# Kernel tuning notes

Measured on AMD Instinct MI355X. Metric: run time of the kernel, lower is better.

The kernel has to match this reference:

```python
import jax, jax.numpy as jnp
import numpy as np

N_RNA, N_DIS = 40000, 3000
E_EDGES, T = 600000, 10000
RNA_IN, D_FEAT, HID, EXP_D = 512, 256, 512, 256
N_EXP, HEADS = 8, 8
HD = HID // HEADS          # per-head dim inside HANConv
MHA_HD = EXP_D // HEADS    # per-head dim in cross-attention
FUSION = 2 * HID


def setup_inputs() -> dict:
    key = jax.random.key(0)
    ks = iter(jax.random.split(key, 48))
    def nrm(shape, s=0.02):
        return jax.random.normal(next(ks), shape, dtype=jnp.float32) * s
    inp = {
        "x_rna": jax.random.normal(next(ks), (N_RNA, RNA_IN), dtype=jnp.float32),
        "x_dis": jax.random.normal(next(ks), (N_DIS, D_FEAT), dtype=jnp.float32),
        "Wd": nrm((RNA_IN, D_FEAT)), "bd": jnp.zeros((RNA_IN,), jnp.float32),
        "Wp_r": nrm((HID, RNA_IN)), "bp_r": jnp.zeros((HID,), jnp.float32),
        "Wp_d": nrm((HID, RNA_IN)), "bp_d": jnp.zeros((HID,), jnp.float32),
        "a_src_rd": nrm((HEADS, HD), 0.1), "a_dst_rd": nrm((HEADS, HD), 0.1),
        "a_src_dr": nrm((HEADS, HD), 0.1), "a_dst_dr": nrm((HEADS, HD), 0.1),
        "kW": nrm((HID, HID)), "kb": jnp.zeros((HID,), jnp.float32),
        "qv": nrm((HID,), 0.1),
        "Wl": nrm((HID, HID)), "bl": jnp.zeros((HID,), jnp.float32),
        "W_exp": nrm((N_EXP, FUSION, EXP_D)), "b_exp": jnp.zeros((N_EXP, EXP_D), jnp.float32),
        "W_gate": nrm((4, HID, N_EXP)),
        "W_head": nrm((4, 2 * EXP_D, EXP_D)), "b_head": jnp.zeros((4, EXP_D), jnp.float32),
        "in_w": nrm((3 * EXP_D, EXP_D)), "in_b": jnp.zeros((3 * EXP_D,), jnp.float32),
        "out_w": nrm((EXP_D, EXP_D)), "out_b": jnp.zeros((EXP_D,), jnp.float32),
        "Wdp": nrm((EXP_D, HID)), "bdp": jnp.zeros((EXP_D,), jnp.float32),
        "ei_rd_src": jax.random.randint(next(ks), (E_EDGES,), 0, N_RNA),
        "ei_rd_dst": jax.random.randint(next(ks), (E_EDGES,), 0, N_DIS),
        "ei_dr_src": jax.random.randint(next(ks), (E_EDGES,), 0, N_DIS),
        "ei_dr_dst": jax.random.randint(next(ks), (E_EDGES,), 0, N_RNA),
        "idx_rels": jax.random.randint(next(ks), (4, T), 0, N_RNA),
    }
    return inp


def _han_edge(x_src, x_dst, ei_src, ei_dst, a_src, a_dst, n_dst):
    # x_*: [N, H, D]; GAT-style attention with softmax per destination node (PyG HANConv edge step)
    as_ = (x_src * a_src).sum(-1)                                 # [Ns, H]
    ad_ = (x_dst * a_dst).sum(-1)                                 # [Nd, H]
    alpha = jax.nn.leaky_relu(as_[ei_src] + ad_[ei_dst], 0.2)     # [E, H]
    amax = jax.ops.segment_max(alpha, ei_dst, num_segments=n_dst)
    ex = jnp.exp(alpha - amax[ei_dst])
    den = jax.ops.segment_sum(ex, ei_dst, num_segments=n_dst)
    w = ex / (den[ei_dst] + 1e-16)
    msg = x_src[ei_src] * w[:, :, None]                           # [E, H, D]
    out = jax.ops.segment_sum(msg, ei_dst, num_segments=n_dst)    # [Nd, H, D]
    return jax.nn.relu(out.reshape(n_dst, -1))


def _semantic(outs, kW, kb, qv):
    # outs: [M, N, F]; metapath-level (semantic) attention from HANConv
    s = (jnp.tanh(outs @ kW.T + kb).mean(axis=1) * qv).sum(-1)    # [M]
    beta = jax.nn.softmax(s)
    return (beta[:, None, None] * outs).sum(0)


def reference(x_rna, x_dis, Wd, bd, Wp_r, bp_r, Wp_d, bp_d,
              a_src_rd, a_dst_rd, a_src_dr, a_dst_dr,
              kW, kb, qv, Wl, bl, W_exp, b_exp, W_gate, W_head, b_head,
              in_w, in_b, out_w, out_b, Wdp, bdp,
              ei_rd_src, ei_rd_dst, ei_dr_src, ei_dr_dst, idx_rels):
    # ---- HAN encoder ----
    xd = x_dis @ Wd.T + bd                                        # disease feat -> rna_in_dim
    hr0 = (x_rna @ Wp_r.T + bp_r).reshape(N_RNA, HEADS, HD)
    hd0 = (xd @ Wp_d.T + bp_d).reshape(N_DIS, HEADS, HD)
    out_dis = _han_edge(hr0, hd0, ei_rd_src, ei_rd_dst, a_src_rd, a_dst_rd, N_DIS)
    out_rna = _han_edge(hd0, hr0, ei_dr_src, ei_dr_dst, a_src_dr, a_dst_dr, N_RNA)
    h_rna = _semantic(out_rna[None], kW, kb, qv) @ Wl.T + bl      # shared final lin
    h_dis = _semantic(out_dis[None], kW, kb, qv) @ Wl.T + bl
    # ---- MoE with per-relation gating ----
    d_global = h_dis.mean(axis=0)
    fusion = jnp.concatenate([h_rna, jnp.broadcast_to(d_global, h_rna.shape)], axis=1)  # [N, 2H]
    E = jax.nn.relu(jnp.einsum('nf,efd->ned', fusion, W_exp) + b_exp)  # [N, Nexp, Ed]
    h_t = h_rna[idx_rels]                                         # [4, T, H]
    scores = jnp.einsum('rth,rhe->rte', h_t, W_gate)              # raw gate scores (no softmax)
    u = (E[idx_rels] * scores[..., None]).sum(axis=2)             # [4, T, Ed]
    U = u.mean(axis=1)                                            # [4, Ed]
    # ---- cross attention over 4 task tokens ----
    qkv = U @ in_w.T + in_b
    q, k, v = jnp.split(qkv, 3, axis=-1)
    def heads(z):
        return z.reshape(4, HEADS, MHA_HD).transpose(1, 0, 2)     # [H, 4, dh]
    qh, kh, vh = heads(q), heads(k), heads(v)
    attn = jax.nn.softmax(jnp.einsum('htd,hsd->hts', qh, kh) / np.float32(np.sqrt(MHA_HD)), axis=-1)
    o = jnp.einsum('hts,hsd->htd', attn, vh).transpose(1, 0, 2).reshape(4, EXP_D)
    U_prime = o @ out_w.T + out_b                                 # [4, Ed]
    # ---- per-relation heads and disease scores ----
    cross = jnp.broadcast_to(U_prime[:, None, :], u.shape)
    cat = jnp.concatenate([u, cross], axis=-1)                    # [4, T, 2Ed]
    p = jax.nn.relu(jnp.einsum('rtc,rcd->rtd', cat, W_head) + b_head[:, None, :])
    d_proj = h_dis @ Wdp.T + bdp                                  # [Ndis, Ed]
    return jax.nn.sigmoid(jnp.einsum('rtd,md->rtm', p, d_proj))   # [4, T, Ndis]
```

## Files before the change

### kernel.cpp

```cpp
#include <hip/hip_runtime.h>
#include <math.h>

constexpr int NRNA = 40000;
constexpr int NDIS = 3000;
constexpr int NEDG = 600000;
constexpr int TREL = 10000;

typedef __attribute__((ext_vector_type(8))) short bh8;
typedef __attribute__((ext_vector_type(4))) float f32x4;

__device__ inline float bf2f(ushort x) {
    union { uint u; float f; } v; v.u = ((uint)x) << 16; return v.f;
}
__device__ inline ushort f2bf(float f) {
    union { float f; uint u; } v; v.f = f;
    uint u = v.u;
    uint r = (u + 0x7fffu + ((u >> 16) & 1u)) >> 16;
    return (ushort)r;
}
__device__ inline float bflo(uint w) { union { uint u; float f; } v; v.u = w << 16; return v.f; }
__device__ inline float bfhi(uint w) { union { uint u; float f; } v; v.u = w & 0xffff0000u; return v.f; }

__device__ inline void gload16(const ushort* g, ushort* l) {
    __builtin_amdgcn_global_load_lds(
        (const __attribute__((address_space(1))) unsigned int*)(const void*)g,
        (__attribute__((address_space(3))) unsigned int*)(void*)l, 16, 0, 0);
}

__device__ inline int xcd_swz(int f, int n) {
    int q = n >> 3, r = n & 7, xcd = f & 7, i = f >> 3;
    return (xcd < r) ? (xcd * (q + 1) + i) : (r * (q + 1) + (xcd - r) * q + i);
}

__global__ __launch_bounds__(256) void conv_bf16(const float* __restrict__ in,
                                                 ushort* __restrict__ out, long n)
{
    long g = ((long)blockIdx.x * 256 + threadIdx.x) * 4;
    if (g >= n) return;
    float4 v = *(const float4*)(in + g);
    ushort4 o;
    o.x = f2bf(v.x); o.y = f2bf(v.y); o.z = f2bf(v.z); o.w = f2bf(v.w);
    *(ushort4*)(out + g) = o;
}

__global__ __launch_bounds__(256) void transpose_bf16(
    const float* __restrict__ in, ushort* __restrict__ out,
    int R, int C, long sIn, long sOut)
{
    __shared__ float t[64][65];
    const int tid = threadIdx.x;
    const int r0 = blockIdx.y * 64, c0 = blockIdx.x * 64;
    const float* ib = in + (long)blockIdx.z * sIn;
    ushort* ob = out + (long)blockIdx.z * sOut;
#pragma unroll
    for (int k = 0; k < 16; ++k) {
        int idx = k * 256 + tid, i = idx >> 6, j = idx & 63;
        t[i][j] = ib[(long)(r0 + i) * C + c0 + j];
    }
    __syncthreads();
#pragma unroll
    for (int k = 0; k < 16; ++k) {
        int idx = k * 256 + tid, i = idx >> 6, j = idx & 63;
        ob[(long)(c0 + i) * R + r0 + j] = f2bf(t[j][i]);
    }
}

__global__ void transpose_wgate(const float* __restrict__ W, float* __restrict__ out)
{
    int g = blockIdx.x * 256 + threadIdx.x;
    int r = g >> 12, e = (g >> 9) & 7, k = g & 511;
    out[g] = W[(long)r * 4096 + (long)k * 8 + e];
}

template<int ACT, bool SWZ>
__global__ __launch_bounds__(256) void gemm_mfma(
    const ushort* __restrict__ A, const ushort* __restrict__ B,
    const float* __restrict__ bias, float* __restrict__ Cf, ushort* __restrict__ Cb,
    const int* __restrict__ idx,
    int M, int N, int K, long sA, long sB, long sBias, long sC)
{
    __shared__ ushort smem[16384];
    ushort* As = smem;
    ushort* Bs = smem + 8192;
    int bx = blockIdx.x, by = blockIdx.y;
    if (SWZ) {
        int n = gridDim.x * gridDim.y;
        int s = xcd_swz(by * gridDim.x + bx, n);
        bx = s % gridDim.x; by = s / gridDim.x;
    }
    const int bz = blockIdx.z;
    const ushort* Ab = A + (long)bz * sA;
    const ushort* Bb = B + (long)bz * sB;
    const float* biasb = bias ? (bias + (long)bz * sBias) : nullptr;
    const int row0 = by * 128, col0 = bx * 128;

    const int tid = threadIdx.x, wid = tid >> 6, lane = tid & 63;
    const int wr = wid >> 1, wc = wid & 1;

    const int lrow = lane >> 3;
    const int lk = (((lane & 7) ^ lrow) * 8);
    const ushort* ap0[4]; const ushort* bp0[4];
    ushort* la[4]; ushort* lb[4];
#pragma unroll
    for (int i = 0; i < 4; ++i) {
        int c = wid * 4 + i;
        int ra = row0 + c * 8 + lrow; ra = ra < M ? ra : M - 1;
        int rs = idx ? idx[ra] : ra;
        ap0[i] = Ab + (long)rs * K + lk;
        int cb = col0 + c * 8 + lrow; cb = cb < N ? cb : N - 1;
        bp0[i] = Bb + (long)cb * K + lk;
        la[i] = As + c * 512;
        lb[i] = Bs + c * 512;
    }

    f32x4 acc[4][4];
#pragma unroll
    for (int i = 0; i < 4; ++i)
#pragma unroll
        for (int n = 0; n < 4; ++n) acc[i][n] = (f32x4){0.f, 0.f, 0.f, 0.f};

    const int fr = lane & 15, fq = lane >> 4;
    const int sw0 = (fq ^ (fr & 7)) * 8;
    const ushort* paRow = As + (wr * 64 + fr) * 64;
    const ushort* pbRow = Bs + (wc * 64 + fr) * 64;

    for (int k0 = 0; k0 < K; k0 += 64) {
#pragma unroll
        for (int i = 0; i < 4; ++i) gload16(ap0[i] + k0, la[i]);
#pragma unroll
        for (int i = 0; i < 4; ++i) gload16(bp0[i] + k0, lb[i]);
        __syncthreads();
#pragma unroll
        for (int kk = 0; kk < 2; ++kk) {
            const int sw = kk ? (sw0 ^ 32) : sw0;
            bh8 af[4], bf[4];
#pragma unroll
            for (int i = 0; i < 4; ++i) af[i] = *(const bh8*)(paRow + i * 1024 + sw);
#pragma unroll
            for (int n = 0; n < 4; ++n) bf[n] = *(const bh8*)(pbRow + n * 1024 + sw);
#pragma unroll
            for (int i = 0; i < 4; ++i)
#pragma unroll
                for (int n = 0; n < 4; ++n)
                    acc[i][n] = __builtin_amdgcn_mfma_f32_16x16x32_bf16(af[i], bf[n], acc[i][n], 0, 0, 0);
        }
        __syncthreads();
    }

    float* cs = (float*)smem;
#pragma unroll
    for (int H = 0; H < 2; ++H) {
        if (wc == H) {
#pragma unroll
            for (int i = 0; i < 4; ++i)
#pragma unroll
                for (int n = 0; n < 4; ++n)
#pragma unroll
                    for (int r = 0; r < 4; ++r)
                        cs[(wr * 64 + i * 16 + fq * 4 + r) * 64 + n * 16 + fr] = acc[i][n][r];
        }
        __syncthreads();
#pragma unroll
        for (int it = 0; it < 8; ++it) {
            int rl = it * 16 + (tid >> 4);
            int cl = (tid & 15) * 4;
            int m = row0 + rl, col = col0 + H * 64 + cl;
            if (m < M && col < N) {
                f32x4 v = *(const f32x4*)(cs + rl * 64 + cl);
                if (biasb) {
                    float4 bv = *(const float4*)(biasb + col);
                    v[0] += bv.x; v[1] += bv.y; v[2] += bv.z; v[3] += bv.w;
                }
                if (ACT == 1) {
#pragma unroll
                    for (int q = 0; q < 4; ++q) v[q] = fmaxf(v[q], 0.f);
                } else if (ACT == 2) {
#pragma unroll
                    for (int q = 0; q < 4; ++q) v[q] = 1.f / (1.f + __expf(-v[q]));
                }
                long o = (long)bz * sC + (long)m * N + col;
                if (Cf) *(f32x4*)(Cf + o) = v;
                if (Cb) {
                    ushort4 ob;
                    ob.x = f2bf(v[0]); ob.y = f2bf(v[1]); ob.z = f2bf(v[2]); ob.w = f2bf(v[3]);
                    *(ushort4*)(Cb + o) = ob;
                }
            }
        }
        __syncthreads();
    }
}

__global__ __launch_bounds__(256) void moe_mfma(
    const ushort* __restrict__ h, const ushort* __restrict__ WexpT,
    const float* __restrict__ c_exp, const float* __restrict__ S,
    const int* __restrict__ idx, ushort* __restrict__ up)
{
    __shared__ ushort smem[24576];
    __shared__ float sS[128 * 2];
    __shared__ float sC[2 * 128];
    ushort* As  = smem;
    ushort* Bs0 = smem + 8192;
    ushort* Bs1 = smem + 16384;
    int bx = blockIdx.x, by = blockIdx.y;
    {
        int n = gridDim.x * gridDim.y;
        int s = xcd_swz(by * gridDim.x + bx, n);
        bx = s % gridDim.x; by = s / gridDim.x;
    }
    const int row0 = by * 128, col0 = bx * 128;
    const int z = blockIdx.z, e0 = z * 2;
    const int tid = threadIdx.x, wid = tid >> 6, lane = tid & 63;
    const int wr = wid >> 1, wc = wid & 1;
    constexpr int M = 4 * TREL;

    {
        int rr = tid >> 1, e = tid & 1;
        sS[tid] = S[(long)(row0 + rr) * 8 + e0 + e];
        int ee = tid >> 7, cc = tid & 127;
        sC[tid] = c_exp[(e0 + ee) * 256 + col0 + cc];
    }

    const int lrow = lane >> 3;
    const int lk = (((lane & 7) ^ lrow) * 8);
    const ushort* ap0[4]; const ushort* bp0[4];
    ushort* la[4]; ushort* lb0[4]; ushort* lb1[4];
#pragma unroll
    for (int i = 0; i < 4; ++i) {
        int c = wid * 4 + i;
        int ra = row0 + c * 8 + lrow;
        ap0[i] = h + (long)idx[ra] * 512 + lk;
        bp0[i] = WexpT + (long)(col0 + c * 8 + lrow) * 512 + (long)e0 * 131072 + lk;
        la[i]  = As  + c * 512;
        lb0[i] = Bs0 + c * 512;
        lb1[i] = Bs1 + c * 512;
    }

    const int fr = lane & 15, fq = lane >> 4;
    const int sw0 = (fq ^ (fr & 7)) * 8;
    const ushort* paRow  = As  + (wr * 64 + fr) * 64;
    const ushort* pb0Row = Bs0 + (wc * 64 + fr) * 64;
    const ushort* pb1Row = Bs1 + (wc * 64 + fr) * 64;

    f32x4 acc0[4][4], acc1[4][4];
#pragma unroll
    for (int i = 0; i < 4; ++i)
#pragma unroll
        for (int n = 0; n < 4; ++n) {
            acc0[i][n] = (f32x4){0.f, 0.f, 0.f, 0.f};
            acc1[i][n] = (f32x4){0.f, 0.f, 0.f, 0.f};
        }
    __syncthreads();

    for (int k0 = 0; k0 < 512; k0 += 64) {
#pragma unroll
        for (int i = 0; i < 4; ++i) gload16(ap0[i] + k0, la[i]);
#pragma unroll
        for (int i = 0; i < 4; ++i) gload16(bp0[i] + k0, lb0[i]);
#pragma unroll
        for (int i = 0; i < 4; ++i) gload16(bp0[i] + 131072 + k0, lb1[i]);
        __syncthreads();
#pragma unroll
        for (int kk = 0; kk < 2; ++kk) {
            const int sw = kk ? (sw0 ^ 32) : sw0;
            bh8 af[4], b0[4], b1[4];
#pragma unroll
            for (int i = 0; i < 4; ++i) af[i] = *(const bh8*)(paRow + i * 1024 + sw);
#pragma unroll
            for (int n = 0; n < 4; ++n) b0[n] = *(const bh8*)(pb0Row + n * 1024 + sw);
#pragma unroll
            for (int n = 0; n < 4; ++n) b1[n] = *(const bh8*)(pb1Row + n * 1024 + sw);
#pragma unroll
            for (int i = 0; i < 4; ++i)
#pragma unroll
                for (int n = 0; n < 4; ++n) {
                    acc0[i][n] = __builtin_amdgcn_mfma_f32_16x16x32_bf16(af[i], b0[n], acc0[i][n], 0, 0, 0);
                    acc1[i][n] = __builtin_amdgcn_mfma_f32_16x16x32_bf16(af[i], b1[n], acc1[i][n], 0, 0, 0);
                }
        }
        __syncthreads();
    }

#pragma unroll
    for (int i = 0; i < 4; ++i) {
        int rl = wr * 64 + i * 16 + fq * 4;
#pragma unroll
        for (int n = 0; n < 4; ++n) {
            int cl = wc * 64 + n * 16 + fr;
            float c0 = sC[cl], c1 = sC[128 + cl];
#pragma unroll
            for (int r = 0; r < 4; ++r) {
                float s0 = sS[(rl + r) * 2 + 0];
                float s1 = sS[(rl + r) * 2 + 1];
                acc0[i][n][r] = s0 * fmaxf(acc0[i][n][r] + c0, 0.f)
                              + s1 * fmaxf(acc1[i][n][r] + c1, 0.f);
            }
        }
    }

    float* cs = (float*)smem;
    ushort* upz = up + (long)z * M * 256;
#pragma unroll
    for (int H = 0; H < 2; ++H) {
        if (wc == H) {
#pragma unroll
            for (int i = 0; i < 4; ++i)
#pragma unroll
                for (int n = 0; n < 4; ++n)
#pragma unroll
                    for (int r = 0; r < 4; ++r)
                        cs[(wr * 64 + i * 16 + fq * 4 + r) * 64 + n * 16 + fr] = acc0[i][n][r];
        }
        __syncthreads();
#pragma unroll
        for (int it = 0; it < 8; ++it) {
            int rl = it * 16 + (tid >> 4);
            int cl = (tid & 15) * 4;
            f32x4 v = *(const f32x4*)(cs + rl * 64 + cl);
            int m = row0 + rl, col = col0 + H * 64 + cl;
            ushort4 ob;
            ob.x = f2bf(v[0]); ob.y = f2bf(v[1]); ob.z = f2bf(v[2]); ob.w = f2bf(v[3]);
            *(ushort4*)(upz + (long)m * 256 + col) = ob;
        }
        __syncthreads();
    }
}

__global__ __launch_bounds__(256) void moe_combine(const ushort* __restrict__ up,
                                                   ushort* __restrict__ u)
{
    constexpr long TOT = (long)4 * TREL * 256;
    long g = ((long)blockIdx.x * 256 + threadIdx.x) * 4;
    if (g >= TOT) return;
    float a[4] = {0.f, 0.f, 0.f, 0.f};
#pragma unroll
    for (int z = 0; z < 4; ++z) {
        ushort4 v = *(const ushort4*)(up + z * TOT + g);
        a[0] += bf2f(v.x); a[1] += bf2f(v.y); a[2] += bf2f(v.z); a[3] += bf2f(v.w);
    }
    ushort4 o;
    o.x = f2bf(a[0]); o.y = f2bf(a[1]); o.z = f2bf(a[2]); o.w = f2bf(a[3]);
    *(ushort4*)(u + g) = o;
}

__global__ void dot_heads_all(const ushort* __restrict__ xr, const ushort* __restrict__ xd,
                              const float* __restrict__ a_src_rd, const float* __restrict__ a_dst_dr,
                              const float* __restrict__ a_dst_rd, const float* __restrict__ a_src_dr,
                              float* __restrict__ as_rd, float* __restrict__ ad_dr,
                              float* __restrict__ ad_rd, float* __restrict__ as_dr)
{
    long g = (long)blockIdx.x * 256 + threadIdx.x;
    const ushort* x; const float *p1, *p2; float *o1, *o2; long gi;
    if (g < (long)NRNA * 8) {
        gi = g; x = xr; p1 = a_src_rd; p2 = a_dst_dr; o1 = as_rd; o2 = ad_dr;
    } else {
        gi = g - (long)NRNA * 8;
        if (gi >= (long)NDIS * 8) return;
        x = xd; p1 = a_dst_rd; p2 = a_src_dr; o1 = ad_rd; o2 = as_dr;
    }
    int node = (int)(gi >> 3), h = (int)(gi & 7);
    const ushort* xp = x + (long)node * 512 + h * 64;
    const float* q1 = p1 + h * 64;
    const float* q2 = p2 + h * 64;
    float s1 = 0.f, s2 = 0.f;
#pragma unroll
    for (int d = 0; d < 64; d += 8) {
        uint4 xv = *(const uint4*)(xp + d);
        float xf[8] = { bflo(xv.x), bfhi(xv.x), bflo(xv.y), bfhi(xv.y),
                        bflo(xv.z), bfhi(xv.z), bflo(xv.w), bfhi(xv.w) };
#pragma unroll
        for (int j = 0; j < 8; ++j) {
            s1 = fmaf(xf[j], q1[d + j], s1);
            s2 = fmaf(xf[j], q2[d + j], s2);
        }
    }
    o1[gi] = s1; o2[gi] = s2;
}

__global__ void hist2(const int* __restrict__ d0, int* __restrict__ deg0,
                      const int* __restrict__ d1, int* __restrict__ deg1, int E)
{
    int g = blockIdx.x * 256 + threadIdx.x;
    if (g >= E) return;
    if (blockIdx.y == 0) atomicAdd(&deg0[d0[g]], 1);
    else                 atomicAdd(&deg1[d1[g]], 1);
}

__global__ __launch_bounds__(1024) void scan_blocks2(
    const int* __restrict__ in0, int* __restrict__ tmp0, int* __restrict__ bs0, int n0,
    const int* __restrict__ in1, int* __restrict__ tmp1, int* __restrict__ bs1, int n1)
{
    const int z = blockIdx.y;
    const int* in = z ? in1 : in0;
    int* tmp = z ? tmp1 : tmp0;
    int* bsum = z ? bs1 : bs0;
    const int n = z ? n1 : n0;
    const int nb = (n + 1023) >> 10;
    if ((int)blockIdx.x >= nb) return;
    __shared__ int wsum[16];
    const int tid = threadIdx.x, lane = tid & 63, wid = tid >> 6;
    int base = blockIdx.x * 1024;
    int v = (base + tid < n) ? in[base + tid] : 0;
    int s = v;
#pragma unroll
    for (int off = 1; off < 64; off <<= 1) {
        int t = __shfl_up(s, off, 64);
        if (lane >= off) s += t;
    }
    if (lane == 63) wsum[wid] = s;
    __syncthreads();
    if (wid == 0) {
        int w = (lane < 16) ? wsum[lane] : 0;
#pragma unroll
        for (int off = 1; off < 16; off <<= 1) {
            int t = __shfl_up(w, off, 64);
            if (lane >= off) w += t;
        }
        if (lane < 16) wsum[lane] = w;
    }
    __syncthreads();
    int incl = s + ((wid == 0) ? 0 : wsum[wid - 1]);
    if (base + tid < n) tmp[base + tid] = incl;
    if (tid == 1023) bsum[blockIdx.x] = incl;
}

__global__ void scan_bsums2(int* __restrict__ bs0, int nb0, int* __restrict__ bs1, int nb1)
{
    int* bsum = blockIdx.x ? bs1 : bs0;
    int nb = blockIdx.x ? nb1 : nb0;
    int lane = threadIdx.x;
    int v = (lane < nb) ? bsum[lane] : 0;
#pragma unroll
    for (int off = 1; off < 64; off <<= 1) {
        int t = __shfl_up(v, off, 64);
        if (lane >= off) v += t;
    }
    if (lane < nb) bsum[lane] = v;
}

__global__ __launch_bounds__(1024) void scan_finish2(
    const int* __restrict__ in0, const int* __restrict__ tmp0, const int* __restrict__ bs0,
    int* __restrict__ offs0, int* __restrict__ cur0, int n0,
    const int* __restrict__ in1, const int* __restrict__ tmp1, const int* __restrict__ bs1,
    int* __restrict__ offs1, int* __restrict__ cur1, int n1)
{
    const int z = blockIdx.y;
    const int* in = z ? in1 : in0;
    const int* tmp = z ? tmp1 : tmp0;
    const int* bsum = z ? bs1 : bs0;
    int* offs = z ? offs1 : offs0;
    int* cur = z ? cur1 : cur0;
    const int n = z ? n1 : n0;
    const int nb = (n + 1023) >> 10;
    if ((int)blockIdx.x >= nb) return;
    int base = blockIdx.x * 1024;
    int i = base + threadIdx.x;
    if (i < n) {
        int pre = (blockIdx.x == 0) ? 0 : bsum[blockIdx.x - 1];
        int v = tmp[i] - in[i] + pre;
        offs[i] = v;
        cur[i] = v;
    }
    if (i == 0) offs[n] = bsum[nb - 1];
}

__global__ void scatter2(const int* __restrict__ s0, const int* __restrict__ d0,
                         int* __restrict__ c0, int* __restrict__ o0,
                         const int* __restrict__ s1, const int* __restrict__ d1,
                         int* __restrict__ c1, int* __restrict__ o1, int E)
{
    int g = blockIdx.x * 256 + threadIdx.x;
    if (g >= E) return;
    if (blockIdx.y == 0) {
        int p = atomicAdd(&c0[d0[g]], 1);
        o0[p] = s0[g];
    } else {
        int p = atomicAdd(&c1[d1[g]], 1);
        o1[p] = s1[g];
    }
}

__global__ __launch_bounds__(256) void han_wave(
    const int* __restrict__ offs, const int* __restrict__ csr_src,
    const float* __restrict__ as_, const float* __restrict__ ad_,
    const ushort* __restrict__ x_src, ushort* __restrict__ out, int nnode)
{
    __shared__ float s_ex[4][64];
    __shared__ int   s_src[4][8];
    __shared__ float s_den[4][8];
    const int w = threadIdx.x >> 6, lane = threadIdx.x & 63;
    const int node = blockIdx.x * 4 + w;
    if (node >= nnode) return;
    const int e0 = offs[node], ne = offs[node + 1] - e0;
    const int myh = lane & 7, grp = lane >> 3;
    const float my_ad = ad_[node * 8 + myh];

    float den = 0.f;
    float acc[8];
#pragma unroll
    for (int k = 0; k < 8; ++k) acc[k] = 0.f;
    const int colbase = lane * 8;

    for (int c0 = 0; c0 < ne; c0 += 8) {
        const int nc = min(8, ne - c0);
        float ex = 0.f;
        int src = 0;
        if (grp < nc) {
            src = csr_src[e0 + c0 + grp];
            float al = as_[(long)src * 8 + myh] + my_ad;
            al = al >= 0.f ? al : 0.2f * al;
            ex = __expf(al);
            den += ex;
        }
        s_ex[w][grp * 8 + myh] = ex;
        if (myh == 0) s_src[w][grp] = src;
        asm volatile("s_waitcnt lgkmcnt(0)" ::: "memory");
        for (int j = 0; j < nc; ++j) {
            float wg = s_ex[w][j * 8 + grp];
            uint4 xv = *(const uint4*)(x_src + (long)s_src[w][j] * 512 + colbase);
            acc[0] = fmaf(wg, bflo(xv.x), acc[0]);
            acc[1] = fmaf(wg, bfhi(xv.x), acc[1]);
            acc[2] = fmaf(wg, bflo(xv.y), acc[2]);
            acc[3] = fmaf(wg, bfhi(xv.y), acc[3]);
            acc[4] = fmaf(wg, bflo(xv.z), acc[4]);
            acc[5] = fmaf(wg, bfhi(xv.z), acc[5]);
            acc[6] = fmaf(wg, bflo(xv.w), acc[6]);
            acc[7] = fmaf(wg, bfhi(xv.w), acc[7]);
        }
        __builtin_amdgcn_wave_barrier();
    }

#pragma unroll
    for (int m = 8; m < 64; m <<= 1) den += __shfl_xor(den, m, 64);
    if (grp == 0) s_den[w][myh] = den;
    asm volatile("s_waitcnt lgkmcnt(0)" ::: "memory");
    float d = s_den[w][grp] + 1e-16f;

    uint4 ov;
    ov.x = (uint)f2bf(fmaxf(acc[0] / d, 0.f)) | ((uint)f2bf(fmaxf(acc[1] / d, 0.f)) << 16);
    ov.y = (uint)f2bf(fmaxf(acc[2] / d, 0.f)) | ((uint)f2bf(fmaxf(acc[3] / d, 0.f)) << 16);
    ov.z = (uint)f2bf(fmaxf(acc[4] / d, 0.f)) | ((uint)f2bf(fmaxf(acc[5] / d, 0.f)) << 16);
    ov.w = (uint)f2bf(fmaxf(acc[6] / d, 0.f)) | ((uint)f2bf(fmaxf(acc[7] / d, 0.f)) << 16);
    *(uint4*)(out + (long)node * 512 + colbase) = ov;
}

__global__ __launch_bounds__(512) void hdis_colsum_partial(const ushort* __restrict__ h_dis,
                                                           float* __restrict__ part)
{
    int c = blockIdx.x, d = threadIdx.x;
    int r0 = c * 200;
    float s = 0.f;
    for (int r = r0; r < r0 + 200; ++r) s += bf2f(h_dis[(long)r * 512 + d]);
    part[c * 512 + d] = s;
}
__global__ __launch_bounds__(512) void hdis_colsum_finish(const float* __restrict__ part,
                                                          float* __restrict__ dg)
{
    int d = threadIdx.x;
    float s = 0.f;
    for (int c = 0; c < 15; ++c) s += part[c * 512 + d];
    dg[d] = s * (1.f / NDIS);
}

__global__ void cexp_part(const float* __restrict__ dg, const float* __restrict__ W_exp,
                          float* __restrict__ part)
{
    int b = blockIdx.x;
    int e = b >> 3, ch = b & 7, d = threadIdx.x;
    const float* W = W_exp + (long)e * 262144 + (long)(512 + ch * 64) * 256 + d;
    float s = 0.f;
    for (int f = 0; f < 64; ++f) s = fmaf(dg[ch * 64 + f], W[(long)f * 256], s);
    part[b * 256 + d] = s;
}
__global__ void cexp_fin(const float* __restrict__ part, const float* __restrict__ b_exp,
                         float* __restrict__ c_exp)
{
    int e = blockIdx.x, d = threadIdx.x;
    float s = b_exp[e * 256 + d];
    for (int ch = 0; ch < 8; ++ch) s += part[(e * 8 + ch) * 256 + d];
    c_exp[e * 256 + d] = s;
}

__global__ __launch_bounds__(256) void scores2(const ushort* __restrict__ h,
                                               const float* __restrict__ WgT,
                                               const int* __restrict__ idx,
                                               float* __restrict__ S)
{
    __shared__ float sW[8 * 512];
    const int r = blockIdx.y;
    const int tid = threadIdx.x;
    for (int i = tid; i < 4096; i += 256) sW[i] = WgT[(long)r * 4096 + i];
    __syncthreads();
    int n = blockIdx.x * 256 + tid;
    if (n >= TREL) return;
    int gi = r * TREL + n;
    const ushort* hp = h + (long)idx[gi] * 512;
    float acc[8];
#pragma unroll
    for (int e = 0; e < 8; ++e) acc[e] = 0.f;
    for (int k = 0; k < 512; k += 8) {
        uint4 hv = *(const uint4*)(hp + k);
        float hf[8];
        hf[0] = bflo(hv.x); hf[1] = bfhi(hv.x); hf[2] = bflo(hv.y); hf[3] = bfhi(hv.y);
        hf[4] = bflo(hv.z); hf[5] = bfhi(hv.z); hf[6] = bflo(hv.w); hf[7] = bfhi(hv.w);
#pragma unroll
        for (int e = 0; e < 8; ++e)
#pragma unroll
            for (int j = 0; j < 8; ++j)
                acc[e] = fmaf(hf[j], sW[e * 512 + k + j], acc[e]);
    }
#pragma unroll
    for (int e = 0; e < 8; ++e) S[(long)gi * 8 + e] = acc[e];
}

__global__ void u_mean_partial(const ushort* __restrict__ u, float* __restrict__ part)
{
    int c = blockIdx.x, r = blockIdx.y, d = threadIdx.x;
    int t0 = c * 313, t1 = min(t0 + 313, TREL);
    const ushort* base = u + ((long)r * TREL) * 256 + d;
    float s = 0.f;
    for (int t = t0; t < t1; ++t) s += bf2f(base[(long)t * 256]);
    part[((long)r * 32 + c) * 256 + d] = s;
}

__global__ __launch_bounds__(256) void tail_kernel(
    const float* __restrict__ u_part,
    const float* __restrict__ in_w, const float* __restrict__ in_b,
    const float* __restrict__ out_w, const float* __restrict__ out_b,
    const float* __restrict__ W_head, const float* __restrict__ b_head,
    float* __restrict__ c_head)
{
    __shared__ float sU[4 * 256];
    __shared__ float sqkv[4 * 768];
    __shared__ float sattn[128];
    __shared__ float so[4 * 256];
    __shared__ float sUp[4 * 256];
    const int tid = threadIdx.x;

    for (int o = tid; o < 1024; o += 256) {
        int r = o >> 8, d = o & 255;
        float s = 0.f;
        for (int c = 0; c < 32; ++c) s += u_part[((long)r * 32 + c) * 256 + d];
        sU[o] = s * (1.f / TREL);
    }
    __syncthreads();

    for (int o = tid; o < 3072; o += 256) {
        int row = o / 768, col = o % 768;
        const float* w = in_w + (long)col * 256;
        const float* uu = sU + row * 256;
        float s = in_b[col];
        for (int k = 0; k < 256; ++k) s = fmaf(uu[k], w[k], s);
        sqkv[o] = s;
    }
    __syncthreads();
    if (tid < 128) {
        int h = tid >> 4, t = (tid >> 2) & 3, s2 = tid & 3;
        const float* q = sqkv + t * 768 + h * 32;
        const float* kk = sqkv + s2 * 768 + 256 + h * 32;
        float s = 0.f;
        for (int d = 0; d < 32; ++d) s += q[d] * kk[d];
        sattn[tid] = s * 0.17677669529663687f;
    }
    __syncthreads();
    if (tid < 32) {
        int base = tid * 4;
        float a0 = sattn[base], a1 = sattn[base+1], a2 = sattn[base+2], a3 = sattn[base+3];
        float m = fmaxf(fmaxf(a0, a1), fmaxf(a2, a3));
        float e0 = __expf(a0 - m), e1 = __expf(a1 - m), e2 = __expf(a2 - m), e3 = __expf(a3 - m);
        float inv = 1.f / (e0 + e1 + e2 + e3);
        sattn[base] = e0 * inv; sattn[base+1] = e1 * inv;
        sattn[base+2] = e2 * inv; sattn[base+3] = e3 * inv;
    }
    __syncthreads();
    for (int o = tid; o < 1024; o += 256) {
        int t = o >> 8, hd = o & 255, h = hd >> 5, d = hd & 31;
        const float* a = sattn + (h * 4 + t) * 4;
        float s = 0.f;
        for (int s2 = 0; s2 < 4; ++s2) s += a[s2] * sqkv[s2 * 768 + 512 + h * 32 + d];
        so[t * 256 + hd] = s;
    }
    __syncthreads();
    for (int o = tid; o < 1024; o += 256) {
        int t = o >> 8, d = o & 255;
        const float* w = out_w + (long)d * 256;
        const float* ov = so + t * 256;
        float s = out_b[d];
        for (int k = 0; k < 256; ++k) s = fmaf(ov[k], w[k], s);
        sUp[o] = s;
    }
    __syncthreads();

    for (int o = tid; o < 1024; o += 256) {
        int r = o >> 8, d = o & 255;
        const float* W = W_head + (long)r * 131072 + 65536 + d;
        const float* up = sUp + r * 256;
        float s = b_head[o];
        for (int c = 0; c < 256; ++c) s = fmaf(up[c], W[(long)c * 256], s);
        c_head[o] = s;
    }
}

extern "C" void kernel_launch(void* const* d_in, const int* in_sizes, int n_in,
                              void* d_out, int out_size, void* d_ws, size_t ws_size,
                              hipStream_t stream)
{
    (void)in_sizes; (void)n_in; (void)out_size;
    const float* x_rna    = (const float*)d_in[0];
    const float* x_dis    = (const float*)d_in[1];
    const float* Wd       = (const float*)d_in[2];
    const float* bd       = (const float*)d_in[3];
    const float* Wp_r     = (const float*)d_in[4];
    const float* bp_r     = (const float*)d_in[5];
    const float* Wp_d     = (const float*)d_in[6];
    const float* bp_d     = (const float*)d_in[7];
    const float* a_src_rd = (const float*)d_in[8];
    const float* a_dst_rd = (const float*)d_in[9];
    const float* a_src_dr = (const float*)d_in[10];
    const float* a_dst_dr = (const float*)d_in[11];
    const float* Wl       = (const float*)d_in[15];
    const float* bl       = (const float*)d_in[16];
    const float* W_exp    = (const float*)d_in[17];
    const float* b_exp    = (const float*)d_in[18];
    const float* W_gate   = (const float*)d_in[19];
    const float* W_head   = (const float*)d_in[20];
    const float* b_head   = (const float*)d_in[21];
    const float* in_w     = (const float*)d_in[22];
    const float* in_b     = (const float*)d_in[23];
    const float* out_w    = (const float*)d_in[24];
    const float* out_b    = (const float*)d_in[25];
    const float* Wdp      = (const float*)d_in[26];
    const float* bdp      = (const float*)d_in[27];
    const int* ei_rd_src  = (const int*)d_in[28];
    const int* ei_rd_dst  = (const int*)d_in[29];
    const int* ei_dr_src  = (const int*)d_in[30];
    const int* ei_dr_dst  = (const int*)d_in[31];
    const int* idx_rels   = (const int*)d_in[32];
    float* out = (float*)d_out;

    char* ws = (char*)d_ws;
    size_t off = 0;
    auto alloc = [&](size_t bytes) -> void* {
        off = (off + 255) & ~(size_t)255;
        void* p = ws + off;
        off += bytes;
        return p;
    };
    constexpr int NALL = NRNA + NDIS;
    ushort* xrb      = (ushort*)alloc((size_t)NRNA * 512 * 2);
    ushort* hr0b     = (ushort*)alloc((size_t)NRNA * 512 * 2);
    ushort* out_all  = (ushort*)alloc((size_t)(NALL + 8) * 512 * 2);
    ushort* h_all    = (ushort*)alloc((size_t)(NALL + 8) * 512 * 2);
    ushort* u_bf     = (ushort*)alloc((size_t)4 * TREL * 256 * 2);
    ushort* p_bf     = (ushort*)alloc((size_t)4 * TREL * 256 * 2);
    ushort* up_bf    = (ushort*)alloc((size_t)4 * 4 * TREL * 256 * 2);
    ushort* xdb      = (ushort*)alloc((size_t)NDIS * 256 * 2);
    ushort* xd_bf    = (ushort*)alloc((size_t)NDIS * 512 * 2);
    ushort* hd0b     = (ushort*)alloc((size_t)NDIS * 512 * 2);
    ushort* dproj_b  = (ushort*)alloc((size_t)NDIS * 256 * 2);
    ushort* Wdb    = (ushort*)alloc((size_t)512 * 256 * 2);
    ushort* Wprb   = (ushort*)alloc((size_t)512 * 512 * 2);
    ushort* Wpdb   = (ushort*)alloc((size_t)512 * 512 * 2);
    ushort* Wlb    = (ushort*)alloc((size_t)512 * 512 * 2);
    ushort* Wdpb   = (ushort*)alloc((size_t)256 * 512 * 2);
    ushort* WexpT  = (ushort*)alloc((size_t)8 * 256 * 512 * 2);
    ushort* WheadT = (ushort*)alloc((size_t)4 * 256 * 256 * 2);
    float*  WgT    = (float*)alloc((size_t)4 * 8 * 512 * 4);
    float* as_rd   = (float*)alloc((size_t)NRNA * 8 * 4);
    float* ad_rd   = (float*)alloc((size_t)NDIS * 8 * 4);
    float* as_dr   = (float*)alloc((size_t)NDIS * 8 * 4);
    float* ad_dr   = (float*)alloc((size_t)NRNA * 8 * 4);
    float* S       = (float*)alloc((size_t)4 * TREL * 8 * 4);
    float* dg_part = (float*)alloc((size_t)15 * 512 * 4);
    float* dg      = (float*)alloc((size_t)512 * 4);
    float* c_exp   = (float*)alloc((size_t)8 * 256 * 4);
    float* ce_part = (float*)alloc((size_t)64 * 256 * 4);
    float* u_part  = (float*)alloc((size_t)4 * 32 * 256 * 4);
    float* c_head  = (float*)alloc((size_t)4 * 256 * 4);
    int* deg_all  = (int*)alloc((size_t)(NDIS + NRNA) * 4);
    int* deg_rd = deg_all, * deg_dr = deg_all + NDIS;
    int* offs_rd = (int*)alloc((size_t)(NDIS + 1) * 4);
    int* cur_rd  = (int*)alloc((size_t)NDIS * 4);
    int* csr_rd  = (int*)alloc((size_t)NEDG * 4);
    int* offs_dr = (int*)alloc((size_t)(NRNA + 1) * 4);
    int* cur_dr  = (int*)alloc((size_t)NRNA * 4);
    int* csr_dr  = (int*)alloc((size_t)NEDG * 4);
    int* tmp_rd  = (int*)alloc((size_t)NDIS * 4);
    int* tmp_dr  = (int*)alloc((size_t)NRNA * 4);
    int* bs_rd   = (int*)alloc((size_t)64 * 4);
    int* bs_dr   = (int*)alloc((size_t)64 * 4);
    if (off > ws_size) return;

    ushort* out_rna = out_all;
    ushort* out_dis = out_all + (size_t)NRNA * 512;
    ushort* h_rna   = h_all;
    ushort* h_dis   = h_all + (size_t)NRNA * 512;

    const dim3 blk(256);

    conv_bf16<<<dim3(20000), blk, 0, stream>>>(x_rna, xrb, (long)NRNA * 512);
    conv_bf16<<<dim3(750),   blk, 0, stream>>>(x_dis, xdb, (long)NDIS * 256);
    conv_bf16<<<dim3(128),   blk, 0, stream>>>(Wd,   Wdb,  512 * 256);
    conv_bf16<<<dim3(256),   blk, 0, stream>>>(Wp_r, Wprb, 512 * 512);
    conv_bf16<<<dim3(256),   blk, 0, stream>>>(Wp_d, Wpdb, 512 * 512);
    conv_bf16<<<dim3(256),   blk, 0, stream>>>(Wl,   Wlb,  512 * 512);
    conv_bf16<<<dim3(128),   blk, 0, stream>>>(Wdp,  Wdpb, 256 * 512);
    transpose_bf16<<<dim3(4, 8, 8), blk, 0, stream>>>(W_exp, WexpT, 512, 256,
                                                      (long)1024 * 256, (long)256 * 512);
    transpose_bf16<<<dim3(4, 4, 4), blk, 0, stream>>>(W_head, WheadT, 256, 256,
                                                      (long)512 * 256, (long)256 * 256);
    transpose_wgate<<<dim3(64), blk, 0, stream>>>(W_gate, WgT);

    gemm_mfma<0,false><<<dim3(4, 24), blk, 0, stream>>>(
        xdb, Wdb, bd, nullptr, xd_bf, nullptr, NDIS, 512, 256, 0, 0, 0, 0);
    gemm_mfma<0,true><<<dim3(4, 313), blk, 0, stream>>>(
        xrb, Wprb, bp_r, nullptr, hr0b, nullptr, NRNA, 512, 512, 0, 0, 0, 0);
    gemm_mfma<0,false><<<dim3(4, 24), blk, 0, stream>>>(
        xd_bf, Wpdb, bp_d, nullptr, hd0b, nullptr, NDIS, 512, 512, 0, 0, 0, 0);

    dot_heads_all<<<dim3(((NRNA + NDIS) * 8 + 255) / 256), blk, 0, stream>>>(
        hr0b, hd0b, a_src_rd, a_dst_dr, a_dst_rd, a_src_dr, as_rd, ad_dr, ad_rd, as_dr);

    hipMemsetAsync(deg_all, 0, (size_t)(NDIS + NRNA) * 4, stream);
    hist2<<<dim3((NEDG + 255) / 256, 2), blk, 0, stream>>>(ei_rd_dst, deg_rd, ei_dr_dst, deg_dr, NEDG);
    scan_blocks2<<<dim3(40, 2), dim3(1024), 0, stream>>>(deg_rd, tmp_rd, bs_rd, NDIS,
                                                         deg_dr, tmp_dr, bs_dr, NRNA);
    scan_bsums2<<<dim3(2), dim3(64), 0, stream>>>(bs_rd, 3, bs_dr, 40);
    scan_finish2<<<dim3(40, 2), dim3(1024), 0, stream>>>(deg_rd, tmp_rd, bs_rd, offs_rd, cur_rd, NDIS,
                                                         deg_dr, tmp_dr, bs_dr, offs_dr, cur_dr, NRNA);
    scatter2<<<dim3((NEDG + 255) / 256, 2), blk, 0, stream>>>(
        ei_rd_src, ei_rd_dst, cur_rd, csr_rd, ei_dr_src, ei_dr_dst, cur_dr, csr_dr, NEDG);

    han_wave<<<dim3((NDIS + 3) / 4), blk, 0, stream>>>(offs_rd, csr_rd, as_rd, ad_rd, hr0b, out_dis, NDIS);
    han_wave<<<dim3(NRNA / 4), blk, 0, stream>>>(offs_dr, csr_dr, as_dr, ad_dr, hd0b, out_rna, NRNA);

    gemm_mfma<0,true><<<dim3(4, (NALL + 127) / 128), blk, 0, stream>>>(
        out_all, Wlb, bl, nullptr, h_all, nullptr, NALL, 512, 512, 0, 0, 0, 0);

    hdis_colsum_partial<<<dim3(15), dim3(512), 0, stream>>>(h_dis, dg_part);
    hdis_colsum_finish<<<dim3(1), dim3(512), 0, stream>>>(dg_part, dg);
    cexp_part<<<dim3(64), blk, 0, stream>>>(dg, W_exp, ce_part);
    cexp_fin<<<dim3(8), blk, 0, stream>>>(ce_part, b_exp, c_exp);
    scores2<<<dim3(40, 4), blk, 0, stream>>>(h_rna, WgT, idx_rels, S);

    moe_mfma<<<dim3(2, 320, 4), blk, 0, stream>>>(h_rna, WexpT, c_exp, S, idx_rels, up_bf);
    moe_combine<<<dim3(10240), blk, 0, stream>>>(up_bf, u_bf);

    u_mean_partial<<<dim3(32, 4), blk, 0, stream>>>(u_bf, u_part);
    tail_kernel<<<dim3(1), blk, 0, stream>>>(u_part, in_w, in_b, out_w, out_b,
                                             W_head, b_head, c_head);

    gemm_mfma<1,false><<<dim3(2, 79, 4), blk, 0, stream>>>(
        u_bf, WheadT, c_head, nullptr, p_bf, nullptr, TREL, 256, 256,
        (long)TREL * 256, 65536, 256, (long)TREL * 256);

    gemm_mfma<0,false><<<dim3(2, 24), blk, 0, stream>>>(
        h_dis, Wdpb, bdp, nullptr, dproj_b, nullptr, NDIS, 256, 512, 0, 0, 0, 0);

    gemm_mfma<2,true><<<dim3(24, 320), blk, 0, stream>>>(
        p_bf, dproj_b, nullptr, out, nullptr, nullptr, 4 * TREL, NDIS, 256, 0, 0, 0, 0);
}
```

Baseline: 1.271 ms.

## Merge small launches and fold disease linear layers into one weight

Several small kernels are merged into single launches: the six fp32-to-bf16 conversions, the two HAN aggregation passes, the gate scores with the disease column sums, and the relation-head GEMM with the disease projection GEMM. The two chained disease linear layers are algebraically folded into one precomputed 512x256 weight plus a combined bias, so the disease projection runs over K=256 once instead of two GEMMs. The aim is to cut launch overhead and small-kernel tail waste. The cost is branchy block dispatch and extra bf16 rounding on the folded weight.

```diff
diff --git a/kernel.cpp b/kernel.cpp
--- a/kernel.cpp
+++ b/kernel.cpp
@@ -32,15 +32,25 @@
     return (xcd < r) ? (xcd * (q + 1) + i) : (r * (q + 1) + (xcd - r) * q + i);
 }
 
-__global__ __launch_bounds__(256) void conv_bf16(const float* __restrict__ in,
-                                                 ushort* __restrict__ out, long n)
-{
-    long g = ((long)blockIdx.x * 256 + threadIdx.x) * 4;
-    if (g >= n) return;
-    float4 v = *(const float4*)(in + g);
+__global__ __launch_bounds__(256) void conv_multi(
+    const float* s0, ushort* d0, const float* s1, ushort* d1,
+    const float* s2, ushort* d2, const float* s3, ushort* d3,
+    const float* s4, ushort* d4, const float* s5, ushort* d5,
+    int c0, int c1, int c2, int c3, int c4, int c5)
+{
+    int b = blockIdx.x;
+    const float* src; ushort* dst; int base;
+    if      (b < c0) { src = s0; dst = d0; base = 0;  }
+    else if (b < c1) { src = s1; dst = d1; base = c0; }
+    else if (b < c2) { src = s2; dst = d2; base = c1; }
+    else if (b < c3) { src = s3; dst = d3; base = c2; }
+    else if (b < c4) { src = s4; dst = d4; base = c3; }
+    else             { src = s5; dst = d5; base = c4; }
+    long g = ((long)(b - base) * 256 + threadIdx.x) * 4;
+    float4 v = *(const float4*)(src + g);
     ushort4 o;
     o.x = f2bf(v.x); o.y = f2bf(v.y); o.z = f2bf(v.z); o.w = f2bf(v.w);
-    *(ushort4*)(out + g) = o;
+    *(ushort4*)(dst + g) = o;
 }
 
 __global__ __launch_bounds__(256) void transpose_bf16(
@@ -72,23 +82,28 @@
     out[g] = W[(long)r * 4096 + (long)k * 8 + e];
 }
 
-template<int ACT, bool SWZ>
-__global__ __launch_bounds__(256) void gemm_mfma(
+__global__ __launch_bounds__(256) void bias_fold(
+    const float* __restrict__ Wp_d, const float* __restrict__ bd,
+    const float* __restrict__ bp_d, float* __restrict__ bias_comb)
+{
+    int p = blockIdx.x * 256 + threadIdx.x;
+    const float* W = Wp_d + (long)p * 512;
+    float s = bp_d[p];
+    for (int o = 0; o < 512; ++o) s = fmaf(W[o], bd[o], s);
+    bias_comb[p] = s;
+}
+
+template<int ACT>
+__device__ inline void gemm_body(
+    ushort* smem,
     const ushort* __restrict__ A, const ushort* __restrict__ B,
     const float* __restrict__ bias, float* __restrict__ Cf, ushort* __restrict__ Cb,
     const int* __restrict__ idx,
-    int M, int N, int K, long sA, long sB, long sBias, long sC)
-{
-    __shared__ ushort smem[16384];
+    int M, int N, int K, long sA, long sB, long sBias, long sC,
+    int bx, int by, int bz)
+{
     ushort* As = smem;
     ushort* Bs = smem + 8192;
-    int bx = blockIdx.x, by = blockIdx.y;
-    if (SWZ) {
-        int n = gridDim.x * gridDim.y;
-        int s = xcd_swz(by * gridDim.x + bx, n);
-        bx = s % gridDim.x; by = s / gridDim.x;
-    }
-    const int bz = blockIdx.z;
     const ushort* Ab = A + (long)bz * sA;
     const ushort* Bb = B + (long)bz * sB;
     const float* biasb = bias ? (bias + (long)bz * sBias) : nullptr;
@@ -188,6 +203,43 @@
             }
         }
         __syncthreads();
+    }
+}
+
+template<int ACT, bool SWZ>
+__global__ __launch_bounds__(256) void gemm_mfma(
+    const ushort* __restrict__ A, const ushort* __restrict__ B,
+    const float* __restrict__ bias, float* __restrict__ Cf, ushort* __restrict__ Cb,
+    const int* __restrict__ idx,
+    int M, int N, int K, long sA, long sB, long sBias, long sC)
+{
+    __shared__ ushort smem[16384];
+    int bx = blockIdx.x, by = blockIdx.y;
+    if (SWZ) {
+        int n = gridDim.x * gridDim.y;
+        int s = xcd_swz(by * gridDim.x + bx, n);
+        bx = s % gridDim.x; by = s / gridDim.x;
+    }
+    gemm_body<ACT>(smem, A, B, bias, Cf, Cb, idx, M, N, K, sA, sB, sBias, sC,
+                   bx, by, blockIdx.z);
+}
+
+__global__ __launch_bounds__(256) void gemm_two(
+    const ushort* __restrict__ u, const ushort* __restrict__ WheadT,
+    const float* __restrict__ c_head, ushort* __restrict__ p,
+    const ushort* __restrict__ h_dis, const ushort* __restrict__ Wdpb,
+    const float* __restrict__ bdp, ushort* __restrict__ dproj)
+{
+    __shared__ ushort smem[16384];
+    const int z = blockIdx.z;
+    if (z < 4) {
+        gemm_body<1>(smem, u, WheadT, c_head, nullptr, p, nullptr,
+                     TREL, 256, 256, (long)TREL * 256, 65536, 256, (long)TREL * 256,
+                     blockIdx.x, blockIdx.y, z);
+    } else if (blockIdx.y < 24) {
+        gemm_body<0>(smem, h_dis, Wdpb, bdp, nullptr, dproj, nullptr,
+                     NDIS, 256, 512, 0, 0, 0, 0,
+                     blockIdx.x, blockIdx.y, 0);
     }
 }
 
@@ -480,16 +532,28 @@
     }
 }
 
-__global__ __launch_bounds__(256) void han_wave(
-    const int* __restrict__ offs, const int* __restrict__ csr_src,
-    const float* __restrict__ as_, const float* __restrict__ ad_,
-    const ushort* __restrict__ x_src, ushort* __restrict__ out, int nnode)
-{
+__global__ __launch_bounds__(256) void han_both(
+    const int* __restrict__ offs_rd, const int* __restrict__ csr_rd,
+    const float* __restrict__ as_rd, const float* __restrict__ ad_rd,
+    const ushort* __restrict__ x_rd, ushort* __restrict__ out_rd,
+    const int* __restrict__ offs_dr, const int* __restrict__ csr_dr,
+    const float* __restrict__ as_dr, const float* __restrict__ ad_dr,
+    const ushort* __restrict__ x_dr, ushort* __restrict__ out_dr)
+{
+    constexpr int NB_RD = (NDIS + 3) / 4;
     __shared__ float s_ex[4][64];
     __shared__ int   s_src[4][8];
     __shared__ float s_den[4][8];
     const int w = threadIdx.x >> 6, lane = threadIdx.x & 63;
-    const int node = blockIdx.x * 4 + w;
+    const int* offs; const int* csr; const float* as_; const float* ad_;
+    const ushort* x_src; ushort* out; int node, nnode;
+    if ((int)blockIdx.x < NB_RD) {
+        node = blockIdx.x * 4 + w; nnode = NDIS;
+        offs = offs_rd; csr = csr_rd; as_ = as_rd; ad_ = ad_rd; x_src = x_rd; out = out_rd;
+    } else {
+        node = (blockIdx.x - NB_RD) * 4 + w; nnode = NRNA;
+        offs = offs_dr; csr = csr_dr; as_ = as_dr; ad_ = ad_dr; x_src = x_dr; out = out_dr;
+    }
     if (node >= nnode) return;
     const int e0 = offs[node], ne = offs[node + 1] - e0;
     const int myh = lane & 7, grp = lane >> 3;
@@ -506,7 +570,7 @@
         float ex = 0.f;
         int src = 0;
         if (grp < nc) {
-            src = csr_src[e0 + c0 + grp];
+            src = csr[e0 + c0 + grp];
             float al = as_[(long)src * 8 + myh] + my_ad;
             al = al >= 0.f ? al : 0.2f * al;
             ex = __expf(al);
@@ -544,21 +608,56 @@
     *(uint4*)(out + (long)node * 512 + colbase) = ov;
 }
 
-__global__ __launch_bounds__(512) void hdis_colsum_partial(const ushort* __restrict__ h_dis,
-                                                           float* __restrict__ part)
-{
-    int c = blockIdx.x, d = threadIdx.x;
-    int r0 = c * 200;
-    float s = 0.f;
-    for (int r = r0; r < r0 + 200; ++r) s += bf2f(h_dis[(long)r * 512 + d]);
-    part[c * 512 + d] = s;
-}
+__global__ __launch_bounds__(256) void scores_colsum(
+    const ushort* __restrict__ h, const float* __restrict__ WgT,
+    const int* __restrict__ idx, float* __restrict__ S,
+    const ushort* __restrict__ h_dis, float* __restrict__ dg_part)
+{
+    const int r = blockIdx.y;
+    const int tid = threadIdx.x;
+    if ((int)blockIdx.x >= 40) {
+        int chunk = r * 4 + (blockIdx.x - 40);
+        int r0 = chunk * 188, r1 = min(r0 + 188, NDIS);
+        float s0 = 0.f, s1 = 0.f;
+        for (int row = r0; row < r1; ++row) {
+            s0 += bf2f(h_dis[(long)row * 512 + tid]);
+            s1 += bf2f(h_dis[(long)row * 512 + tid + 256]);
+        }
+        dg_part[chunk * 512 + tid] = s0;
+        dg_part[chunk * 512 + 256 + tid] = s1;
+        return;
+    }
+    __shared__ float sW[8 * 512];
+    for (int i = tid; i < 4096; i += 256) sW[i] = WgT[(long)r * 4096 + i];
+    __syncthreads();
+    int n = blockIdx.x * 256 + tid;
+    if (n >= TREL) return;
+    int gi = r * TREL + n;
+    const ushort* hp = h + (long)idx[gi] * 512;
+    float acc[8];
+#pragma unroll
+    for (int e = 0; e < 8; ++e) acc[e] = 0.f;
+    for (int k = 0; k < 512; k += 8) {
+        uint4 hv = *(const uint4*)(hp + k);
+        float hf[8];
+        hf[0] = bflo(hv.x); hf[1] = bfhi(hv.x); hf[2] = bflo(hv.y); hf[3] = bfhi(hv.y);
+        hf[4] = bflo(hv.z); hf[5] = bfhi(hv.z); hf[6] = bflo(hv.w); hf[7] = bfhi(hv.w);
+#pragma unroll
+        for (int e = 0; e < 8; ++e)
+#pragma unroll
+            for (int j = 0; j < 8; ++j)
+                acc[e] = fmaf(hf[j], sW[e * 512 + k + j], acc[e]);
+    }
+#pragma unroll
+    for (int e = 0; e < 8; ++e) S[(long)gi * 8 + e] = acc[e];
+}
+
 __global__ __launch_bounds__(512) void hdis_colsum_finish(const float* __restrict__ part,
                                                           float* __restrict__ dg)
 {
     int d = threadIdx.x;
     float s = 0.f;
-    for (int c = 0; c < 15; ++c) s += part[c * 512 + d];
+    for (int c = 0; c < 16; ++c) s += part[c * 512 + d];
     dg[d] = s * (1.f / NDIS);
 }
 
@@ -579,38 +678,6 @@
     float s = b_exp[e * 256 + d];
     for (int ch = 0; ch < 8; ++ch) s += part[(e * 8 + ch) * 256 + d];
     c_exp[e * 256 + d] = s;
-}
-
-__global__ __launch_bounds__(256) void scores2(const ushort* __restrict__ h,
-                                               const float* __restrict__ WgT,
-                                               const int* __restrict__ idx,
-                                               float* __restrict__ S)
-{
-    __shared__ float sW[8 * 512];
-    const int r = blockIdx.y;
-    const int tid = threadIdx.x;
-    for (int i = tid; i < 4096; i += 256) sW[i] = WgT[(long)r * 4096 + i];
-    __syncthreads();
-    int n = blockIdx.x * 256 + tid;
-    if (n >= TREL) return;
-    int gi = r * TREL + n;
-    const ushort* hp = h + (long)idx[gi] * 512;
-    float acc[8];
-#pragma unroll
-    for (int e = 0; e < 8; ++e) acc[e] = 0.f;
-    for (int k = 0; k < 512; k += 8) {
-        uint4 hv = *(const uint4*)(hp + k);
-        float hf[8];
-        hf[0] = bflo(hv.x); hf[1] = bfhi(hv.x); hf[2] = bflo(hv.y); hf[3] = bfhi(hv.y);
-        hf[4] = bflo(hv.z); hf[5] = bfhi(hv.z); hf[6] = bflo(hv.w); hf[7] = bfhi(hv.w);
-#pragma unroll
-        for (int e = 0; e < 8; ++e)
-#pragma unroll
-            for (int j = 0; j < 8; ++j)
-                acc[e] = fmaf(hf[j], sW[e * 512 + k + j], acc[e]);
-    }
-#pragma unroll
-    for (int e = 0; e < 8; ++e) S[(long)gi * 8 + e] = acc[e];
 }
 
 __global__ void u_mean_partial(const ushort* __restrict__ u, float* __restrict__ part)
@@ -755,23 +822,24 @@
     ushort* p_bf     = (ushort*)alloc((size_t)4 * TREL * 256 * 2);
     ushort* up_bf    = (ushort*)alloc((size_t)4 * 4 * TREL * 256 * 2);
     ushort* xdb      = (ushort*)alloc((size_t)NDIS * 256 * 2);
-    ushort* xd_bf    = (ushort*)alloc((size_t)NDIS * 512 * 2);
     ushort* hd0b     = (ushort*)alloc((size_t)NDIS * 512 * 2);
     ushort* dproj_b  = (ushort*)alloc((size_t)NDIS * 256 * 2);
-    ushort* Wdb    = (ushort*)alloc((size_t)512 * 256 * 2);
     ushort* Wprb   = (ushort*)alloc((size_t)512 * 512 * 2);
     ushort* Wpdb   = (ushort*)alloc((size_t)512 * 512 * 2);
     ushort* Wlb    = (ushort*)alloc((size_t)512 * 512 * 2);
     ushort* Wdpb   = (ushort*)alloc((size_t)256 * 512 * 2);
+    ushort* WdTb   = (ushort*)alloc((size_t)256 * 512 * 2);
+    ushort* Wc_bf  = (ushort*)alloc((size_t)512 * 256 * 2);
     ushort* WexpT  = (ushort*)alloc((size_t)8 * 256 * 512 * 2);
     ushort* WheadT = (ushort*)alloc((size_t)4 * 256 * 256 * 2);
     float*  WgT    = (float*)alloc((size_t)4 * 8 * 512 * 4);
+    float* bias_c  = (float*)alloc((size_t)512 * 4);
     float* as_rd   = (float*)alloc((size_t)NRNA * 8 * 4);
     float* ad_rd   = (float*)alloc((size_t)NDIS * 8 * 4);
     float* as_dr   = (float*)alloc((size_t)NDIS * 8 * 4);
     float* ad_dr   = (float*)alloc((size_t)NRNA * 8 * 4);
     float* S       = (float*)alloc((size_t)4 * TREL * 8 * 4);
-    float* dg_part = (float*)alloc((size_t)15 * 512 * 4);
+    float* dg_part = (float*)alloc((size_t)16 * 512 * 4);
     float* dg      = (float*)alloc((size_t)512 * 4);
     float* c_exp   = (float*)alloc((size_t)8 * 256 * 4);
     float* ce_part = (float*)alloc((size_t)64 * 256 * 4);
@@ -798,25 +866,24 @@
 
     const dim3 blk(256);
 
-    conv_bf16<<<dim3(20000), blk, 0, stream>>>(x_rna, xrb, (long)NRNA * 512);
-    conv_bf16<<<dim3(750),   blk, 0, stream>>>(x_dis, xdb, (long)NDIS * 256);
-    conv_bf16<<<dim3(128),   blk, 0, stream>>>(Wd,   Wdb,  512 * 256);
-    conv_bf16<<<dim3(256),   blk, 0, stream>>>(Wp_r, Wprb, 512 * 512);
-    conv_bf16<<<dim3(256),   blk, 0, stream>>>(Wp_d, Wpdb, 512 * 512);
-    conv_bf16<<<dim3(256),   blk, 0, stream>>>(Wl,   Wlb,  512 * 512);
-    conv_bf16<<<dim3(128),   blk, 0, stream>>>(Wdp,  Wdpb, 256 * 512);
+    conv_multi<<<dim3(21646), blk, 0, stream>>>(
+        x_rna, xrb, x_dis, xdb, Wp_r, Wprb, Wp_d, Wpdb, Wl, Wlb, Wdp, Wdpb,
+        20000, 20750, 21006, 21262, 21518, 21646);
     transpose_bf16<<<dim3(4, 8, 8), blk, 0, stream>>>(W_exp, WexpT, 512, 256,
                                                       (long)1024 * 256, (long)256 * 512);
     transpose_bf16<<<dim3(4, 4, 4), blk, 0, stream>>>(W_head, WheadT, 256, 256,
                                                       (long)512 * 256, (long)256 * 256);
+    transpose_bf16<<<dim3(4, 8, 1), blk, 0, stream>>>(Wd, WdTb, 512, 256, 0, 0);
     transpose_wgate<<<dim3(64), blk, 0, stream>>>(W_gate, WgT);
-
-    gemm_mfma<0,false><<<dim3(4, 24), blk, 0, stream>>>(
-        xdb, Wdb, bd, nullptr, xd_bf, nullptr, NDIS, 512, 256, 0, 0, 0, 0);
+    bias_fold<<<dim3(2), blk, 0, stream>>>(Wp_d, bd, bp_d, bias_c);
+
+    gemm_mfma<0,false><<<dim3(2, 4), blk, 0, stream>>>(
+        Wpdb, WdTb, nullptr, nullptr, Wc_bf, nullptr, 512, 256, 512, 0, 0, 0, 0);
+
     gemm_mfma<0,true><<<dim3(4, 313), blk, 0, stream>>>(
         xrb, Wprb, bp_r, nullptr, hr0b, nullptr, NRNA, 512, 512, 0, 0, 0, 0);
     gemm_mfma<0,false><<<dim3(4, 24), blk, 0, stream>>>(
-        xd_bf, Wpdb, bp_d, nullptr, hd0b, nullptr, NDIS, 512, 512, 0, 0, 0, 0);
+        xdb, Wc_bf, bias_c, nullptr, hd0b, nullptr, NDIS, 512, 256, 0, 0, 0, 0);
 
     dot_heads_all<<<dim3(((NRNA + NDIS) * 8 + 255) / 256), blk, 0, stream>>>(
         hr0b, hd0b, a_src_rd, a_dst_dr, a_dst_rd, a_src_dr, as_rd, ad_dr, ad_rd, as_dr);
@@ -831,17 +898,17 @@
     scatter2<<<dim3((NEDG + 255) / 256, 2), blk, 0, stream>>>(
         ei_rd_src, ei_rd_dst, cur_rd, csr_rd, ei_dr_src, ei_dr_dst, cur_dr, csr_dr, NEDG);
 
-    han_wave<<<dim3((NDIS + 3) / 4), blk, 0, stream>>>(offs_rd, csr_rd, as_rd, ad_rd, hr0b, out_dis, NDIS);
-    han_wave<<<dim3(NRNA / 4), blk, 0, stream>>>(offs_dr, csr_dr, as_dr, ad_dr, hd0b, out_rna, NRNA);
+    han_both<<<dim3((NDIS + 3) / 4 + NRNA / 4), blk, 0, stream>>>(
+        offs_rd, csr_rd, as_rd, ad_rd, hr0b, out_dis,
+        offs_dr, csr_dr, as_dr, ad_dr, hd0b, out_rna);
 
     gemm_mfma<0,true><<<dim3(4, (NALL + 127) / 128), blk, 0, stream>>>(
         out_all, Wlb, bl, nullptr, h_all, nullptr, NALL, 512, 512, 0, 0, 0, 0);
 
-    hdis_colsum_partial<<<dim3(15), dim3(512), 0, stream>>>(h_dis, dg_part);
+    scores_colsum<<<dim3(44, 4), blk, 0, stream>>>(h_rna, WgT, idx_rels, S, h_dis, dg_part);
     hdis_colsum_finish<<<dim3(1), dim3(512), 0, stream>>>(dg_part, dg);
     cexp_part<<<dim3(64), blk, 0, stream>>>(dg, W_exp, ce_part);
     cexp_fin<<<dim3(8), blk, 0, stream>>>(ce_part, b_exp, c_exp);
-    scores2<<<dim3(40, 4), blk, 0, stream>>>(h_rna, WgT, idx_rels, S);
 
     moe_mfma<<<dim3(2, 320, 4), blk, 0, stream>>>(h_rna, WexpT, c_exp, S, idx_rels, up_bf);
     moe_combine<<<dim3(10240), blk, 0, stream>>>(up_bf, u_bf);
@@ -850,12 +917,8 @@
     tail_kernel<<<dim3(1), blk, 0, stream>>>(u_part, in_w, in_b, out_w, out_b,
                                              W_head, b_head, c_head);
 
-    gemm_mfma<1,false><<<dim3(2, 79, 4), blk, 0, stream>>>(
-        u_bf, WheadT, c_head, nullptr, p_bf, nullptr, TREL, 256, 256,
-        (long)TREL * 256, 65536, 256, (long)TREL * 256);
-
-    gemm_mfma<0,false><<<dim3(2, 24), blk, 0, stream>>>(
-        h_dis, Wdpb, bdp, nullptr, dproj_b, nullptr, NDIS, 256, 512, 0, 0, 0, 0);
+    gemm_two<<<dim3(2, 79, 5), blk, 0, stream>>>(
+        u_bf, WheadT, c_head, p_bf, h_dis, Wdpb, bdp, dproj_b);
 
     gemm_mfma<2,true><<<dim3(24, 320), blk, 0, stream>>>(
         p_bf, dproj_b, nullptr, out, nullptr, nullptr, 4 * TREL, NDIS, 256, 0, 0, 0, 0);
```

Measured after the change: 1.377 ms. 1.08x slower.
